# Optimization experiments

Measured on AMD Instinct MI355X. Metric: run time of the kernel, lower is better.

## Reference

```python
import jax, jax.numpy as jnp
import numpy as np

B, T, D, UNITS = 64, 512, 512, 512  # batch, time, input dim, GRU units (output_size, unidirectional)


def setup_inputs() -> dict:
    key = jax.random.key(0)
    ks = jax.random.split(key, 8)
    s = 0.05
    x = jax.random.normal(ks[0], (B, T, D), jnp.float32)
    lengths = jax.random.randint(ks[1], (B,), T // 4, T + 1)
    mask = jnp.arange(T)[None, :] < lengths[:, None]  # [B, T] bool, contiguous valid prefix
    # Keras GRUCell (reset_after=True): kernel [in,3u], recurrent_kernel [u,3u], bias [2,3u] (input/recurrent)
    W0 = jax.random.normal(ks[2], (D, 3 * UNITS), jnp.float32) * s
    U0 = jax.random.normal(ks[3], (UNITS, 3 * UNITS), jnp.float32) * s
    b0 = jnp.zeros((2, 3 * UNITS), jnp.float32)
    W1 = jax.random.normal(ks[4], (UNITS, 3 * UNITS), jnp.float32) * s
    U1 = jax.random.normal(ks[5], (UNITS, 3 * UNITS), jnp.float32) * s
    b1 = jnp.zeros((2, 3 * UNITS), jnp.float32)
    return {"x": x, "mask": mask, "W0": W0, "U0": U0, "b0": b0, "W1": W1, "U1": U1, "b1": b1}


def _gru_cell(h, xt, W, U, b):
    # Keras GRU v2 math (reset_after=True), gate order [z, r, h]
    gi = xt @ W + b[0]
    gh = h @ U + b[1]
    iz, ir, ih = jnp.split(gi, 3, axis=-1)
    hz, hr, hh = jnp.split(gh, 3, axis=-1)
    z = jax.nn.sigmoid(iz + hz)
    r = jax.nn.sigmoid(ir + hr)
    cand = jnp.tanh(ih + r * hh)
    return z * h + (1.0 - z) * cand


def reference(x, mask, W0, U0, b0, W1, U1, b1):
    b = x.shape[0]
    units = U0.shape[0]
    h0 = jnp.zeros((b, units), x.dtype)
    h1 = jnp.zeros((b, units), x.dtype)
    out0 = jnp.zeros((b, units), x.dtype)

    def step(carry, inp):
        h0, h1, prev_out = carry
        xt, mt = inp
        m = mt[:, None]
        # StackedRNNCells: layer-1 sees layer-0's raw output; masking applied to states/output afterwards
        h0n = _gru_cell(h0, xt, W0, U0, b0)
        h1n = _gru_cell(h1, h0n, W1, U1, b1)
        h0c = jnp.where(m, h0n, h0)
        h1c = jnp.where(m, h1n, h1)
        out = jnp.where(m, h1n, prev_out)  # keras.backend.rnn repeats previous output on masked steps
        return (h0c, h1c, out), out

    (h0f, h1f, _), outs = jax.lax.scan(
        step, (h0, h1, out0), (jnp.swapaxes(x, 0, 1), jnp.swapaxes(mask, 0, 1))
    )
    output = jnp.swapaxes(outs, 0, 1)  # [B, T, units]
    return output, h0f, h1f
```

## Files before the change

### kernel.cpp

```cpp
#include <hip/hip_runtime.h>
#include <stdint.h>


#define TT 512

typedef __attribute__((ext_vector_type(8))) short bfrag_t;
typedef __attribute__((ext_vector_type(4))) float f32x4;

__device__ inline unsigned short f2bf(float f) {
  unsigned u = __float_as_uint(f);
  unsigned r = u + 0x7FFFu + ((u >> 16) & 1u);
  return (unsigned short)(r >> 16);
}
__device__ inline unsigned pack2(float lo, float hi) {
  return (unsigned)f2bf(lo) | ((unsigned)f2bf(hi) << 16);
}
__device__ inline float sigmoidf_(float x) { return 1.0f / (1.0f + __expf(-x)); }
__device__ inline float fast_tanh(float x) {
  float ax = fabsf(x);
  float e = __expf(-2.0f * ax);
  float t = (1.0f - e) / (1.0f + e);
  return x < 0.0f ? -t : t;
}

__device__ inline void st8(void* p, unsigned long long v) {
  __hip_atomic_store((unsigned long long*)p, v, __ATOMIC_RELAXED, __HIP_MEMORY_SCOPE_AGENT);
}
__device__ inline unsigned long long ld8(const void* p) {
  return __hip_atomic_load((const unsigned long long*)p, __ATOMIC_RELAXED, __HIP_MEMORY_SCOPE_AGENT);
}

__device__ inline void spingroup(const unsigned* f, unsigned expect) {
  const unsigned* p = f + (threadIdx.x & 63);
  for (;;) {
    unsigned v = __hip_atomic_load(p, __ATOMIC_RELAXED, __HIP_MEMORY_SCOPE_AGENT);
    if (__ballot(v == expect) == 0xFFFFFFFFFFFFFFFFull) break;
  }
}

extern "C" __global__ void __launch_bounds__(256, 1)
gru2_lockstep(const float* __restrict__ x,
              const int*   __restrict__ mask,
              const float* __restrict__ W0,
              const float* __restrict__ U0,
              const float* __restrict__ b0,
              const float* __restrict__ W1,
              const float* __restrict__ U1,
              const float* __restrict__ b1,
              float* __restrict__ out,
              unsigned char* __restrict__ ws)
{
  extern __shared__ unsigned short sm[];
  unsigned short* wt  = sm;
  unsigned short* st0 = sm + 96 * 520;
  unsigned short* st1 = st0 + 16 * 520;
  float* accs = (float*)(st1 + 16 * 520);
  unsigned short* pub16 = (unsigned short*)(accs + 1024);

  unsigned short* h0pub = (unsigned short*)ws;
  unsigned short* h1pub = (unsigned short*)(ws + 131072);
  unsigned short* h0n   = (unsigned short*)(ws + 262144);
  unsigned*       flags = (unsigned*)      (ws + 393216);

  const int tid  = threadIdx.x;
  const int wg   = blockIdx.x;
  const int pipe = wg & 1;
  const int idx  = wg >> 1;
  const int mi = idx & 3,  ni = idx >> 2;
  const int r0 = mi * 16,  c0 = ni * 16;
  const int member = (ni << 1) | pipe;
  const int wave = tid >> 6, lane = tid & 63;
  const int quad = lane >> 4, n16 = lane & 15;

  const float* Wm = pipe ? W1 : W0;
  const float* Um = pipe ? U1 : U0;
  const float* bp = pipe ? b1 : b0;
  unsigned short* hpub = pipe ? h1pub : h0pub;

  {
    const int col  = tid & 15;
    const int ksub = tid >> 4;
    for (int k0 = 0; k0 < 512; k0 += 16) {
      const int k = k0 + ksub;
      const float* M0 = Wm + (size_t)k * 1536;
      const float* M1 = Um + (size_t)k * 1536;
      #pragma unroll
      for (int g = 0; g < 3; ++g) {
        wt[(g * 16 + col) * 520 + k]      = f2bf(M0[g * 512 + c0 + col]);
        wt[(48 + g * 16 + col) * 520 + k] = f2bf(M1[g * 512 + c0 + col]);
      }
    }
  }
  __syncthreads();

  const int g  = (wave < 2) ? wave : 2;
  const int np = (wave < 2) ? 2 : 1;

  bfrag_t bw0[16], bw1[16];
  {
    const int mat0 = (wave == 3) ? 1 : 0;
    const int row0 = mat0 * 48 + g * 16 + n16;
    #pragma unroll
    for (int f = 0; f < 16; ++f)
      bw0[f] = *(const bfrag_t*)&wt[row0 * 520 + f * 32 + quad * 8];
    if (np == 2) {
      const int row1 = 48 + g * 16 + n16;
      #pragma unroll
      for (int f = 0; f < 16; ++f)
        bw1[f] = *(const bfrag_t*)&wt[row1 * 520 + f * 32 + quad * 8];
    }
  }

  float bsc;
  {
    const int colg = g * 512 + c0 + n16;
    const float bi = bp[colg];
    const float bh = bp[1536 + colg];
    bsc = (wave < 2) ? (bi + bh) : ((wave == 2) ? bi : bh);
  }

  float hcar = 0.0f;
  float oprev = 0.0f;
  const int erow = tid >> 4, ecol = tid & 15;
  const int eb = r0 + erow, ec = c0 + ecol;

  for (int s = 0; s <= TT; ++s) {
    const bool actA = (pipe == 0) && (s < TT);
    const bool actB = (pipe == 1) && (s > 0);
    const bool act  = actA || actB;
    const int  t    = pipe ? (s - 1) : s;

    const int mv = act ? mask[(size_t)eb * 512 + t] : 0;

    if (actA && tid >= 128) {
      const int sm2 = (tid - 128) >> 3;
      const int sk2 = (tid & 7) * 64;
      const float* src = x + (((size_t)(r0 + sm2) * 512 + s) * 512 + sk2);
      uint4* dst = (uint4*)(st0 + sm2 * 520 + sk2);
      #pragma unroll
      for (int c = 0; c < 8; ++c) {
        float4 a = ((const float4*)src)[2 * c];
        float4 b = ((const float4*)src)[2 * c + 1];
        uint4 u;
        u.x = pack2(a.x, a.y);  u.y = pack2(a.z, a.w);
        u.z = pack2(b.x, b.y);  u.w = pack2(b.z, b.w);
        dst[c] = u;
      }
    } else if (wave == 0 && s > 0) {
      spingroup(flags + (size_t)(s - 1) * 256 + mi * 64, (unsigned)s);
    }
    __syncthreads();

    if (act) {
      const int row = tid >> 4;
      const int cofs = (tid & 15) * 32;
      const unsigned short* hsrc = hpub + (size_t)((t + 1) & 1) * 32768 +
                                   (size_t)(r0 + row) * 512 + cofs;
      #pragma unroll
      for (int j = 0; j < 8; ++j) {
        unsigned long long v = ld8(hsrc + j * 4);
        *(unsigned long long*)&st1[row * 520 + cofs + j * 4] = v;
      }
      if (pipe == 1) {
        const unsigned short* nsrc = h0n + (size_t)(t & 1) * 32768 +
                                     (size_t)(r0 + row) * 512 + cofs;
        #pragma unroll
        for (int j = 0; j < 8; ++j) {
          unsigned long long v = ld8(nsrc + j * 4);
          *(unsigned long long*)&st0[row * 520 + cofs + j * 4] = v;
        }
      }
    }
    __syncthreads();

    if (act) {
      f32x4 acc = {bsc, bsc, bsc, bsc};
      const unsigned short* s0 = (wave == 3) ? st1 : st0;
      const int abase = n16 * 520 + quad * 8;
      #pragma unroll
      for (int f = 0; f < 16; ++f) {
        bfrag_t a = *(const bfrag_t*)&s0[abase + f * 32];
        acc = __builtin_amdgcn_mfma_f32_16x16x32_bf16(a, bw0[f], acc, 0, 0, 0);
      }
      if (np == 2) {
        #pragma unroll
        for (int f = 0; f < 16; ++f) {
          bfrag_t a = *(const bfrag_t*)&st1[abase + f * 32];
          acc = __builtin_amdgcn_mfma_f32_16x16x32_bf16(a, bw1[f], acc, 0, 0, 0);
        }
      }
      #pragma unroll
      for (int i = 0; i < 4; ++i)
        accs[wave * 256 + (quad * 4 + i) * 16 + n16] = acc[i];
    }
    __syncthreads();

    if (act) {
      const float zv = sigmoidf_(accs[tid]);
      const float rv = sigmoidf_(accs[256 + tid]);
      const float candv = fast_tanh(accs[512 + tid] + rv * accs[768 + tid]);
      const float hold = hcar;
      const float hn = zv * hold + (1.0f - zv) * candv;
      const bool  m  = mv != 0;
      const float hc = m ? hn : hold;
      hcar = hc;
      pub16[erow * 16 + ecol] = f2bf(hc);
      if (pipe == 0) {
        pub16[256 + erow * 16 + ecol] = f2bf(hn);
        if (t == TT - 1) out[(size_t)16777216 + (size_t)eb * 512 + ec] = hc;
      } else {
        const float ov = m ? hn : oprev;
        oprev = ov;
        out[(size_t)eb * 262144 + (size_t)t * 512 + ec] = ov;
        if (t == TT - 1) out[(size_t)16777216 + 32768 + (size_t)eb * 512 + ec] = hc;
      }
    }
    __syncthreads();

    if (act) {
      const int nst = (pipe == 0) ? 128 : 64;
      if (tid < nst) {
        const int v  = tid >> 6;
        const int r  = (tid >> 2) & 15;
        const int sg = tid & 3;
        unsigned long long val = *(unsigned long long*)&pub16[v * 256 + r * 16 + sg * 4];
        unsigned short* dst;
        if (pipe == 0) dst = (v ? h0n : h0pub) + (size_t)(t & 1) * 32768;
        else           dst = h1pub + (size_t)(t & 1) * 32768;
        st8(dst + (size_t)(r0 + r) * 512 + c0 + sg * 4, val);
      }
    }
    asm volatile("s_waitcnt vmcnt(0)" ::: "memory");
    __syncthreads();
    if (tid == 0)
      __hip_atomic_store(&flags[(size_t)s * 256 + mi * 64 + member],
                         (unsigned)(s + 1),
                         __ATOMIC_RELAXED, __HIP_MEMORY_SCOPE_AGENT);
  }
}

extern "C" void kernel_launch(void* const* d_in, const int* in_sizes, int n_in,
                              void* d_out, int out_size, void* d_ws, size_t ws_size,
                              hipStream_t stream) {
  (void)in_sizes; (void)n_in; (void)out_size;
  const float* x    = (const float*)d_in[0];
  const int*   mask = (const int*)  d_in[1];
  const float* W0   = (const float*)d_in[2];
  const float* U0   = (const float*)d_in[3];
  const float* b0   = (const float*)d_in[4];
  const float* W1   = (const float*)d_in[5];
  const float* U1   = (const float*)d_in[6];
  const float* b1   = (const float*)d_in[7];
  float* out = (float*)d_out;
  unsigned char* ws = (unsigned char*)d_ws;

  const size_t need = 918528;
  const size_t zb = ws_size < need ? ws_size : need;
  hipMemsetAsync(d_ws, 0, zb, stream);

  hipFuncSetAttribute((const void*)gru2_lockstep,
                      hipFuncAttributeMaxDynamicSharedMemorySize, 139264);
  void* args[] = { (void*)&x, (void*)&mask, (void*)&W0, (void*)&U0, (void*)&b0,
                   (void*)&W1, (void*)&U1, (void*)&b1, (void*)&out, (void*)&ws };
  hipLaunchCooperativeKernel((void*)gru2_lockstep, dim3(256), dim3(256),
                             args, 139264, stream);
}
```

Baseline: 2.454 ms.

## Split flags per pipe, add XCC-local L2-scope exchange and deeper layer skew

Reworks cross-workgroup synchronisation of the lockstep two-layer GRU. Flags are split per layer pipe into a ring of 4 slots, and each wave spins on only 32 producers. Layer 1 now lags layer 0 by two steps, with h0n quadruple-buffered to match. Each workgroup records its XCC id at startup; when all of its peers share an XCC, h-state exchange uses sc0 (L2-coherent) loads and stores instead of agent-scope atomics. Output stores are moved after the flag publish to take them off the critical path. The costs are a startup handshake, one extra step, and reliance on hardware XCC placement.

```diff
diff --git a/kernel.cpp b/kernel.cpp
--- a/kernel.cpp
+++ b/kernel.cpp
@@ -6,6 +6,7 @@
 
 typedef __attribute__((ext_vector_type(8))) short bfrag_t;
 typedef __attribute__((ext_vector_type(4))) float f32x4;
+typedef __attribute__((ext_vector_type(4))) unsigned uint4v;
 
 __device__ inline unsigned short f2bf(float f) {
   unsigned u = __float_as_uint(f);
@@ -29,12 +30,36 @@
 __device__ inline unsigned long long ld8(const void* p) {
   return __hip_atomic_load((const unsigned long long*)p, __ATOMIC_RELAXED, __HIP_MEMORY_SCOPE_AGENT);
 }
-
-__device__ inline void spingroup(const unsigned* f, unsigned expect) {
-  const unsigned* p = f + (threadIdx.x & 63);
+__device__ inline void st8c(void* p, unsigned long long v, bool l2) {
+  if (l2) asm volatile("global_store_dwordx2 %0, %1, off sc0" :: "v"(p), "v"(v) : "memory");
+  else st8(p, v);
+}
+__device__ inline void ld64c(const void* p, uint4v& a, uint4v& b, uint4v& c, uint4v& d, bool l2) {
+  if (l2) {
+    asm volatile(
+      "global_load_dwordx4 %0, %4, off sc0\n\t"
+      "global_load_dwordx4 %1, %4, off offset:16 sc0\n\t"
+      "global_load_dwordx4 %2, %4, off offset:32 sc0\n\t"
+      "global_load_dwordx4 %3, %4, off offset:48 sc0\n\t"
+      "s_waitcnt vmcnt(0)"
+      : "=&v"(a), "=&v"(b), "=&v"(c), "=&v"(d) : "v"(p) : "memory");
+  } else {
+    const unsigned long long* q = (const unsigned long long*)p;
+    unsigned long long v0 = ld8(q+0), v1 = ld8(q+1), v2 = ld8(q+2), v3 = ld8(q+3);
+    unsigned long long v4 = ld8(q+4), v5 = ld8(q+5), v6 = ld8(q+6), v7 = ld8(q+7);
+    a = uint4v{(unsigned)v0, (unsigned)(v0>>32), (unsigned)v1, (unsigned)(v1>>32)};
+    b = uint4v{(unsigned)v2, (unsigned)(v2>>32), (unsigned)v3, (unsigned)(v3>>32)};
+    c = uint4v{(unsigned)v4, (unsigned)(v4>>32), (unsigned)v5, (unsigned)(v5>>32)};
+    d = uint4v{(unsigned)v6, (unsigned)(v6>>32), (unsigned)v7, (unsigned)(v7>>32)};
+  }
+}
+
+__device__ inline void spin32(const unsigned* f, unsigned expect) {
+  const int lane = threadIdx.x & 63;
+  const unsigned* p = f + (lane & 31);
   for (;;) {
     unsigned v = __hip_atomic_load(p, __ATOMIC_RELAXED, __HIP_MEMORY_SCOPE_AGENT);
-    if (__ballot(v == expect) == 0xFFFFFFFFFFFFFFFFull) break;
+    if (__ballot((v >= expect) || (lane >= 32)) == 0xFFFFFFFFFFFFFFFFull) break;
   }
 }
 
@@ -60,7 +85,8 @@
   unsigned short* h0pub = (unsigned short*)ws;
   unsigned short* h1pub = (unsigned short*)(ws + 131072);
   unsigned short* h0n   = (unsigned short*)(ws + 262144);
-  unsigned*       flags = (unsigned*)      (ws + 393216);
+  unsigned*       xcc   = (unsigned*)      (ws + 524288);
+  unsigned*       flags = (unsigned*)      (ws + 525312);
 
   const int tid  = threadIdx.x;
   const int wg   = blockIdx.x;
@@ -68,7 +94,6 @@
   const int idx  = wg >> 1;
   const int mi = idx & 3,  ni = idx >> 2;
   const int r0 = mi * 16,  c0 = ni * 16;
-  const int member = (ni << 1) | pipe;
   const int wave = tid >> 6, lane = tid & 63;
   const int quad = lane >> 4, n16 = lane & 15;
 
@@ -76,6 +101,11 @@
   const float* Um = pipe ? U1 : U0;
   const float* bp = pipe ? b1 : b0;
   unsigned short* hpub = pipe ? h1pub : h0pub;
+
+  unsigned myx;
+  asm volatile("s_getreg_b32 %0, hwreg(HW_REG_XCC_ID)" : "=s"(myx));
+  if (tid == 0)
+    __hip_atomic_store(&xcc[wg], myx + 1, __ATOMIC_RELAXED, __HIP_MEMORY_SCOPE_AGENT);
 
   {
     const int col  = tid & 15;
@@ -90,6 +120,23 @@
         wt[(48 + g * 16 + col) * 520 + k] = f2bf(M1[g * 512 + c0 + col]);
       }
     }
+  }
+
+  bool loc;
+  {
+    const unsigned* px = xcc + 4 * lane;
+    for (;;) {
+      unsigned a = __hip_atomic_load(px+0, __ATOMIC_RELAXED, __HIP_MEMORY_SCOPE_AGENT);
+      unsigned b = __hip_atomic_load(px+1, __ATOMIC_RELAXED, __HIP_MEMORY_SCOPE_AGENT);
+      unsigned c = __hip_atomic_load(px+2, __ATOMIC_RELAXED, __HIP_MEMORY_SCOPE_AGENT);
+      unsigned d = __hip_atomic_load(px+3, __ATOMIC_RELAXED, __HIP_MEMORY_SCOPE_AGENT);
+      if (__ballot(a && b && c && d) == 0xFFFFFFFFFFFFFFFFull) break;
+    }
+    unsigned ref = myx + 1, peerv = ref;
+    if (lane < 32)
+      peerv = __hip_atomic_load(&xcc[pipe + 2*mi + 8*(lane & 31)],
+                                __ATOMIC_RELAXED, __HIP_MEMORY_SCOPE_AGENT);
+    loc = (__ballot(peerv == ref) == 0xFFFFFFFFFFFFFFFFull);
   }
   __syncthreads();
 
@@ -124,15 +171,15 @@
   const int erow = tid >> 4, ecol = tid & 15;
   const int eb = r0 + erow, ec = c0 + ecol;
 
-  for (int s = 0; s <= TT; ++s) {
+  for (int s = 0; s <= TT + 1; ++s) {
     const bool actA = (pipe == 0) && (s < TT);
-    const bool actB = (pipe == 1) && (s > 0);
+    const bool actB = (pipe == 1) && (s >= 2);
     const bool act  = actA || actB;
-    const int  t    = pipe ? (s - 1) : s;
+    const int  t    = pipe ? (s - 2) : s;
 
     const int mv = act ? mask[(size_t)eb * 512 + t] : 0;
 
-    if (actA && tid >= 128) {
+    if ((pipe == 0) && (s < TT) && tid >= 128) {
       const int sm2 = (tid - 128) >> 3;
       const int sk2 = (tid & 7) * 64;
       const float* src = x + (((size_t)(r0 + sm2) * 512 + s) * 512 + sk2);
@@ -146,29 +193,32 @@
         u.z = pack2(b.x, b.y);  u.w = pack2(b.z, b.w);
         dst[c] = u;
       }
-    } else if (wave == 0 && s > 0) {
-      spingroup(flags + (size_t)(s - 1) * 256 + mi * 64, (unsigned)s);
+    }
+    if (wave == 0 && s > 0) {
+      spin32(flags + ((((s - 1) & 3) * 4 + mi) * 2 + pipe) * 32, (unsigned)s);
+    } else if (wave == 1 && s >= 2) {
+      spin32(flags + ((((s - 2) & 3) * 4 + mi) * 2 + (1 - pipe)) * 32, (unsigned)(s - 1));
     }
     __syncthreads();
 
     if (act) {
       const int row = tid >> 4;
       const int cofs = (tid & 15) * 32;
-      const unsigned short* hsrc = hpub + (size_t)((t + 1) & 1) * 32768 +
-                                   (size_t)(r0 + row) * 512 + cofs;
-      #pragma unroll
-      for (int j = 0; j < 8; ++j) {
-        unsigned long long v = ld8(hsrc + j * 4);
-        *(unsigned long long*)&st1[row * 520 + cofs + j * 4] = v;
-      }
+      const size_t goff = (size_t)(r0 + row) * 512 + cofs;
+      unsigned long long n0=0,n1=0,n2=0,n3=0,n4=0,n5=0,n6=0,n7=0;
       if (pipe == 1) {
-        const unsigned short* nsrc = h0n + (size_t)(t & 1) * 32768 +
-                                     (size_t)(r0 + row) * 512 + cofs;
-        #pragma unroll
-        for (int j = 0; j < 8; ++j) {
-          unsigned long long v = ld8(nsrc + j * 4);
-          *(unsigned long long*)&st0[row * 520 + cofs + j * 4] = v;
-        }
+        const unsigned short* nsrc = h0n + (size_t)(t & 3) * 32768 + goff;
+        n0 = ld8(nsrc + 0);  n1 = ld8(nsrc + 4);  n2 = ld8(nsrc + 8);  n3 = ld8(nsrc + 12);
+        n4 = ld8(nsrc + 16); n5 = ld8(nsrc + 20); n6 = ld8(nsrc + 24); n7 = ld8(nsrc + 28);
+      }
+      uint4v a, b, c, d;
+      ld64c(hpub + (size_t)((t + 1) & 1) * 32768 + goff, a, b, c, d, loc);
+      uint4v* d1 = (uint4v*)&st1[row * 520 + cofs];
+      d1[0] = a; d1[1] = b; d1[2] = c; d1[3] = d;
+      if (pipe == 1) {
+        unsigned long long* d0 = (unsigned long long*)&st0[row * 520 + cofs];
+        d0[0] = n0; d0[1] = n1; d0[2] = n2; d0[3] = n3;
+        d0[4] = n4; d0[5] = n5; d0[6] = n6; d0[7] = n7;
       }
     }
     __syncthreads();
@@ -207,12 +257,8 @@
       pub16[erow * 16 + ecol] = f2bf(hc);
       if (pipe == 0) {
         pub16[256 + erow * 16 + ecol] = f2bf(hn);
-        if (t == TT - 1) out[(size_t)16777216 + (size_t)eb * 512 + ec] = hc;
       } else {
-        const float ov = m ? hn : oprev;
-        oprev = ov;
-        out[(size_t)eb * 262144 + (size_t)t * 512 + ec] = ov;
-        if (t == TT - 1) out[(size_t)16777216 + 32768 + (size_t)eb * 512 + ec] = hc;
+        oprev = m ? hn : oprev;
       }
     }
     __syncthreads();
@@ -224,18 +270,30 @@
         const int r  = (tid >> 2) & 15;
         const int sg = tid & 3;
         unsigned long long val = *(unsigned long long*)&pub16[v * 256 + r * 16 + sg * 4];
-        unsigned short* dst;
-        if (pipe == 0) dst = (v ? h0n : h0pub) + (size_t)(t & 1) * 32768;
-        else           dst = h1pub + (size_t)(t & 1) * 32768;
-        st8(dst + (size_t)(r0 + r) * 512 + c0 + sg * 4, val);
+        const size_t off = (size_t)(r0 + r) * 512 + c0 + sg * 4;
+        if (pipe == 0) {
+          if (v == 0) st8c(h0pub + (size_t)(t & 1) * 32768 + off, val, loc);
+          else        st8 (h0n   + (size_t)(t & 3) * 32768 + off, val);
+        } else {
+          st8c(h1pub + (size_t)(t & 1) * 32768 + off, val, loc);
+        }
       }
     }
     asm volatile("s_waitcnt vmcnt(0)" ::: "memory");
     __syncthreads();
     if (tid == 0)
-      __hip_atomic_store(&flags[(size_t)s * 256 + mi * 64 + member],
+      __hip_atomic_store(flags + (((s & 3) * 4 + mi) * 2 + pipe) * 32 + ni,
                          (unsigned)(s + 1),
                          __ATOMIC_RELAXED, __HIP_MEMORY_SCOPE_AGENT);
+
+    if (act) {
+      if (pipe == 1) {
+        out[(size_t)eb * 262144 + (size_t)t * 512 + ec] = oprev;
+        if (t == TT - 1) out[(size_t)(16777216 + 32768) + (size_t)eb * 512 + ec] = hcar;
+      } else if (t == TT - 1) {
+        out[(size_t)16777216 + (size_t)eb * 512 + ec] = hcar;
+      }
+    }
   }
 }
 
@@ -254,7 +312,7 @@
   float* out = (float*)d_out;
   unsigned char* ws = (unsigned char*)d_ws;
 
-  const size_t need = 918528;
+  const size_t need = 529408;
   const size_t zb = ws_size < need ? ws_size : need;
   hipMemsetAsync(d_ws, 0, zb, stream);
 
```

Result: faster. 2.117 ms (-13.7%).
